# Kernel optimization log

Hardware: AMD Instinct MI355X
Metric: run time of the kernel (lower is better)

Reference implementation:

```python
import jax, jax.numpy as jnp
import numpy as np

B, L, D = 2, 256, 256


def setup_inputs() -> dict:
    key = jax.random.key(0)
    k1, k2, k3, k4 = jax.random.split(key, 4)
    x = jax.random.normal(k1, (B, L, D), dtype=jnp.float32)
    # nn.Linear(dim, 2*dim, bias=False): weight (2*dim, dim), out = x @ W.T
    W_a = jax.random.normal(k2, (2 * D, D), dtype=jnp.float32) / np.sqrt(D).astype(np.float32)
    # last_hidden_init: complex (dim,) parameter, split into real/imag floats
    h0_real = jax.random.normal(k3, (D,), dtype=jnp.float32)
    h0_imag = jax.random.normal(k4, (D,), dtype=jnp.float32)
    return {"x": x, "W_a": W_a, "h0_real": h0_real, "h0_imag": h0_imag}


def reference(x, W_a, h0_real, h0_imag):
    b, l, d = x.shape
    # a = view_as_complex(linear_a(x).float().view(b, l, d, 2))
    raw = (x.astype(jnp.float32) @ W_a.T).reshape(b, l, d, 2)
    re, im = raw[..., 0], raw[..., 1]
    mag2 = re * re + im * im                       # |a|^2
    a = jax.lax.complex(re, im) * (jax.lax.rsqrt(mag2) * jnp.exp(-mag2))
    a_ln = jnp.log(a)                              # (b, l, d) complex
    a_ln = jnp.transpose(a_ln, (0, 2, 1))          # (b, d, l)

    ii = jnp.arange(l)[:, None]
    kk = jnp.arange(l)[None, :]
    # a_ln_tri[b,d,i,k] = a_ln[b,d,k] if k >= i else 0 (== .triu())
    tri = jnp.where(kk >= ii, a_ln[:, :, None, :], 0.0)   # (b, d, l, l)
    # FFT causal conv with ones(len,len) row == cumulative sum along k
    cum = jnp.cumsum(tri, axis=-1)
    # c[b,d,i,k] = exp(sum_{j=i}^{k} a_ln_j) for k>=i, 1 at k=i-1, 0 below (.triu(-1))
    c = jnp.where(kk >= ii - 1, jnp.exp(cum), 0.0)         # (b, d, l, l)

    xT = jnp.transpose(x.astype(jnp.complex64), (0, 2, 1))  # (b, d, l)
    x_hat = jnp.roll(xT, 1, axis=2)                          # x_hat[k] = x[k-1]
    h0 = jax.lax.complex(h0_real, h0_imag)                   # (d,)
    x_hat = x_hat.at[:, :, 0].set(jnp.broadcast_to(h0, (b, d)))
    # x_mat does not depend on i, so (x_mat * c).sum(3) == einsum over k
    h = jnp.einsum('bdik,bdk->bdi', c, x_hat)
    h = h.at[:, :, -1].add(xT[:, :, -1])
    return jnp.transpose(h.real, (0, 2, 1)).astype(x.dtype)  # (b, l, d)
```

## Files before the change

kernel.cpp:

```cpp
#include <hip/hip_runtime.h>
#include <hip/hip_bf16.h>


constexpr int B = 2, L = 256, D = 256, K = 256;
constexpr int LT = 4;

__global__ __launch_bounds__(256) void gemm_a_kernel(
    const float* __restrict__ x,
    const float* __restrict__ W,
    float2* __restrict__ a)
{
    const int blk = blockIdx.x;
    const int b  = blk / (L / LT);
    const int l0 = (blk % (L / LT)) * LT;
    const int d  = threadIdx.x;

    __shared__ float xs[LT][K];

    const float4* src = (const float4*)(x + (size_t)(b * L + l0) * K);
    ((float4*)&xs[0][0])[d] = src[d];
    __syncthreads();

    const float4* w0 = (const float4*)(W + (size_t)(2 * d) * K);
    const float4* w1 = (const float4*)(W + (size_t)(2 * d + 1) * K);

    float accr[LT] = {0.f, 0.f, 0.f, 0.f};
    float acci[LT] = {0.f, 0.f, 0.f, 0.f};

#pragma unroll 4
    for (int k = 0; k < K / 4; ++k) {
        const float4 v0 = w0[k];
        const float4 v1 = w1[k];
#pragma unroll
        for (int r = 0; r < LT; ++r) {
            const float4 xv = ((const float4*)&xs[r][0])[k];
            accr[r] += v0.x * xv.x + v0.y * xv.y + v0.z * xv.z + v0.w * xv.w;
            acci[r] += v1.x * xv.x + v1.y * xv.y + v1.z * xv.z + v1.w * xv.w;
        }
    }

#pragma unroll
    for (int r = 0; r < LT; ++r) {
        const float re = accr[r], im = acci[r];
        const float m2 = re * re + im * im;
        const float s  = rsqrtf(m2) * expf(-m2);
        a[(size_t)(b * L + l0 + r) * D + d] = make_float2(re * s, im * s);
    }
}

__global__ __launch_bounds__(256) void scan_h_kernel(
    const float* __restrict__ x,
    const float2* __restrict__ a,
    const float* __restrict__ h0r,
    const float* __restrict__ h0i,
    float* __restrict__ out)
{
    const int b = blockIdx.x >> 8;
    const int d = blockIdx.x & 255;
    const int i = threadIdx.x;

    __shared__ float2 As[L];
    __shared__ float2 Bs[L];

    const size_t col = (size_t)b * L * D + d;

    const float2 ai = a[col + (size_t)i * D];
    float xr, xi;
    if (i == 0) { xr = h0r[d]; xi = h0i[d]; }
    else        { xr = x[col + (size_t)(i - 1) * D]; xi = 0.f; }

    float Ar = ai.x, Ai = ai.y;
    float Br = ai.x * xr - ai.y * xi;
    float Bi = ai.x * xi + ai.y * xr;

#pragma unroll
    for (int o = 1; o < L; o <<= 1) {
        As[i] = make_float2(Ar, Ai);
        Bs[i] = make_float2(Br, Bi);
        __syncthreads();
        if (i + o < L) {
            const float2 An = As[i + o];
            const float2 Bn = Bs[i + o];
            const float nAr = Ar * An.x - Ai * An.y;
            const float nAi = Ar * An.y + Ai * An.x;
            const float nBr = Ar * Bn.x - Ai * Bn.y + Br;
            const float nBi = Ar * Bn.y + Ai * Bn.x + Bi;
            Ar = nAr; Ai = nAi; Br = nBr; Bi = nBi;
        }
        __syncthreads();
    }

    float o_val = Br;
    if (i >= 2)      o_val += x[col + (size_t)(i - 2) * D];
    else if (i == 1) o_val += h0r[d];
    if (i == L - 1)  o_val += x[col + (size_t)(L - 1) * D];
    out[col + (size_t)i * D] = o_val;
}

extern "C" void kernel_launch(void* const* d_in, const int* in_sizes, int n_in,
                              void* d_out, int out_size, void* d_ws, size_t ws_size,
                              hipStream_t stream) {
    const float* x    = (const float*)d_in[0];
    const float* W_a  = (const float*)d_in[1];
    const float* h0r  = (const float*)d_in[2];
    const float* h0i  = (const float*)d_in[3];
    float* out = (float*)d_out;
    float2* a  = (float2*)d_ws;

    gemm_a_kernel<<<dim3(B * (L / LT)), dim3(256), 0, stream>>>(x, W_a, a);
    scan_h_kernel<<<dim3(B * D), dim3(256), 0, stream>>>(x, a, h0r, h0i, out);
}
```

Before: 82.52 us.

## Retile linear GEMM into 16x16 output tiles with shared-memory W and x

The projection GEMM moves from one thread per output column reading W rows straight from global memory to 2D tiles: each block stages 16 rows of x and 32 rows of W in padded shared memory, and each thread computes one complex output. The grid grows from 128 to 512 blocks, which improves occupancy and removes the uncoalesced per-thread W streaming. In exchange each thread does less register reuse, and shared memory per block rises to about 50KB.

```diff
diff --git a/kernel.cpp b/kernel.cpp
--- a/kernel.cpp
+++ b/kernel.cpp
@@ -3,49 +3,62 @@
 
 
 constexpr int B = 2, L = 256, D = 256, K = 256;
-constexpr int LT = 4;
+constexpr int TL = 16;
+constexpr int TD = 16;
+constexpr int PAD = 260;
 
 __global__ __launch_bounds__(256) void gemm_a_kernel(
     const float* __restrict__ x,
     const float* __restrict__ W,
     float2* __restrict__ a)
 {
-    const int blk = blockIdx.x;
-    const int b  = blk / (L / LT);
-    const int l0 = (blk % (L / LT)) * LT;
-    const int d  = threadIdx.x;
+    const int dt = blockIdx.x;
+    const int lt = blockIdx.y;
+    const int b  = blockIdx.z;
+    const int t  = threadIdx.x;
+    const int l0 = lt * TL;
+    const int d0 = dt * TD;
+    const int r0 = 2 * d0;
 
-    __shared__ float xs[LT][K];
+    __shared__ float xs[TL][PAD];
+    __shared__ float ws[2 * TD][PAD];
 
-    const float4* src = (const float4*)(x + (size_t)(b * L + l0) * K);
-    ((float4*)&xs[0][0])[d] = src[d];
+    {
+        const float4* src = (const float4*)(x + (size_t)(b * L + l0) * K);
+#pragma unroll
+        for (int j = 0; j < 4; ++j) {
+            const int g = j * 256 + t;
+            const int row = g >> 6, c4 = g & 63;
+            *(float4*)&xs[row][c4 * 4] = src[g];
+        }
+    }
+    {
+        const float4* src = (const float4*)(W + (size_t)r0 * K);
+#pragma unroll
+        for (int j = 0; j < 8; ++j) {
+            const int g = j * 256 + t;
+            const int row = g >> 6, c4 = g & 63;
+            *(float4*)&ws[row][c4 * 4] = src[g];
+        }
+    }
     __syncthreads();
 
-    const float4* w0 = (const float4*)(W + (size_t)(2 * d) * K);
-    const float4* w1 = (const float4*)(W + (size_t)(2 * d + 1) * K);
+    const int l  = t >> 4;
+    const int dd = t & 15;
 
-    float accr[LT] = {0.f, 0.f, 0.f, 0.f};
-    float acci[LT] = {0.f, 0.f, 0.f, 0.f};
-
-#pragma unroll 4
-    for (int k = 0; k < K / 4; ++k) {
-        const float4 v0 = w0[k];
-        const float4 v1 = w1[k];
-#pragma unroll
-        for (int r = 0; r < LT; ++r) {
-            const float4 xv = ((const float4*)&xs[r][0])[k];
-            accr[r] += v0.x * xv.x + v0.y * xv.y + v0.z * xv.z + v0.w * xv.w;
-            acci[r] += v1.x * xv.x + v1.y * xv.y + v1.z * xv.z + v1.w * xv.w;
-        }
+    float re = 0.f, im = 0.f;
+#pragma unroll 8
+    for (int k4 = 0; k4 < K / 4; ++k4) {
+        const float4 xv = *(const float4*)&xs[l][k4 * 4];
+        const float4 w0 = *(const float4*)&ws[2 * dd][k4 * 4];
+        const float4 w1 = *(const float4*)&ws[2 * dd + 1][k4 * 4];
+        re += xv.x * w0.x + xv.y * w0.y + xv.z * w0.z + xv.w * w0.w;
+        im += xv.x * w1.x + xv.y * w1.y + xv.z * w1.z + xv.w * w1.w;
     }
 
-#pragma unroll
-    for (int r = 0; r < LT; ++r) {
-        const float re = accr[r], im = acci[r];
-        const float m2 = re * re + im * im;
-        const float s  = rsqrtf(m2) * expf(-m2);
-        a[(size_t)(b * L + l0 + r) * D + d] = make_float2(re * s, im * s);
-    }
+    const float m2 = re * re + im * im;
+    const float s  = rsqrtf(m2) * expf(-m2);
+    a[(size_t)(b * L + l0 + l) * D + d0 + dd] = make_float2(re * s, im * s);
 }
 
 __global__ __launch_bounds__(256) void scan_h_kernel(
@@ -107,6 +120,6 @@
     float* out = (float*)d_out;
     float2* a  = (float2*)d_ws;
 
-    gemm_a_kernel<<<dim3(B * (L / LT)), dim3(256), 0, stream>>>(x, W_a, a);
+    gemm_a_kernel<<<dim3(D / TD, L / TL, B), dim3(256), 0, stream>>>(x, W_a, a);
     scan_h_kernel<<<dim3(B * D), dim3(256), 0, stream>>>(x, a, h0r, h0i, out);
 }
```

Result: faster. 71.87 us (-12.9%).

## Fuse projection GEMM and complex scan into a single kernel

Applied to the files above, without the earlier changes.

Merges the linear projection and the associative complex scan into one kernel. Each 512-thread block computes the projection for two feature columns across all positions, then scans them in shared memory. This removes the workspace round-trip for the intermediate a and one kernel launch, and packs the scan state into one float4 array. In exchange, every thread reads a full row of x from global memory with a stride of K between threads, so x is re-read once per feature pair with no shared tiling. The grid also shrinks to 256 blocks.

```diff
diff --git a/kernel.cpp b/kernel.cpp
--- a/kernel.cpp
+++ b/kernel.cpp
@@ -3,98 +3,72 @@
 
 
 constexpr int B = 2, L = 256, D = 256, K = 256;
-constexpr int LT = 4;
 
-__global__ __launch_bounds__(256) void gemm_a_kernel(
+__global__ __launch_bounds__(512) void sioconv_fused_kernel(
     const float* __restrict__ x,
     const float* __restrict__ W,
-    float2* __restrict__ a)
-{
-    const int blk = blockIdx.x;
-    const int b  = blk / (L / LT);
-    const int l0 = (blk % (L / LT)) * LT;
-    const int d  = threadIdx.x;
-
-    __shared__ float xs[LT][K];
-
-    const float4* src = (const float4*)(x + (size_t)(b * L + l0) * K);
-    ((float4*)&xs[0][0])[d] = src[d];
-    __syncthreads();
-
-    const float4* w0 = (const float4*)(W + (size_t)(2 * d) * K);
-    const float4* w1 = (const float4*)(W + (size_t)(2 * d + 1) * K);
-
-    float accr[LT] = {0.f, 0.f, 0.f, 0.f};
-    float acci[LT] = {0.f, 0.f, 0.f, 0.f};
-
-#pragma unroll 4
-    for (int k = 0; k < K / 4; ++k) {
-        const float4 v0 = w0[k];
-        const float4 v1 = w1[k];
-#pragma unroll
-        for (int r = 0; r < LT; ++r) {
-            const float4 xv = ((const float4*)&xs[r][0])[k];
-            accr[r] += v0.x * xv.x + v0.y * xv.y + v0.z * xv.z + v0.w * xv.w;
-            acci[r] += v1.x * xv.x + v1.y * xv.y + v1.z * xv.z + v1.w * xv.w;
-        }
-    }
-
-#pragma unroll
-    for (int r = 0; r < LT; ++r) {
-        const float re = accr[r], im = acci[r];
-        const float m2 = re * re + im * im;
-        const float s  = rsqrtf(m2) * expf(-m2);
-        a[(size_t)(b * L + l0 + r) * D + d] = make_float2(re * s, im * s);
-    }
-}
-
-__global__ __launch_bounds__(256) void scan_h_kernel(
-    const float* __restrict__ x,
-    const float2* __restrict__ a,
     const float* __restrict__ h0r,
     const float* __restrict__ h0i,
     float* __restrict__ out)
 {
-    const int b = blockIdx.x >> 8;
-    const int d = blockIdx.x & 255;
-    const int i = threadIdx.x;
+    const int b  = blockIdx.x >> 7;
+    const int dp = blockIdx.x & 127;
+    const int t  = threadIdx.x;
+    const int c  = t >> 8;
+    const int l  = t & 255;
+    const int d  = 2 * dp + c;
 
-    __shared__ float2 As[L];
-    __shared__ float2 Bs[L];
+    const float4* x4 = (const float4*)(x + (size_t)(b * L + l) * K);
+    const float4* w4 = (const float4*)(W + (size_t)(2 * d) * K);
 
-    const size_t col = (size_t)b * L * D + d;
+    float re = 0.f, im = 0.f;
+#pragma unroll 8
+    for (int k4 = 0; k4 < K / 4; ++k4) {
+        const float4 xv = x4[k4];
+        const float4 w0 = w4[k4];
+        const float4 w1 = w4[k4 + 64];
+        re += xv.x * w0.x + xv.y * w0.y + xv.z * w0.z + xv.w * w0.w;
+        im += xv.x * w1.x + xv.y * w1.y + xv.z * w1.z + xv.w * w1.w;
+    }
 
-    const float2 ai = a[col + (size_t)i * D];
+    const float m2 = re * re + im * im;
+    const float s  = rsqrtf(m2) * expf(-m2);
+    const float ar = re * s, ai = im * s;
+
+    __shared__ float4 Ms[2][L];
+    __shared__ float  xcol[2][L];
+
+    const size_t colbase = (size_t)b * L * D + d;
+
     float xr, xi;
-    if (i == 0) { xr = h0r[d]; xi = h0i[d]; }
-    else        { xr = x[col + (size_t)(i - 1) * D]; xi = 0.f; }
+    if (l == 0) { xr = h0r[d]; xi = h0i[d]; }
+    else        { xr = x[colbase + (size_t)(l - 1) * D]; xi = 0.f; }
+    xcol[c][l] = xr;
 
-    float Ar = ai.x, Ai = ai.y;
-    float Br = ai.x * xr - ai.y * xi;
-    float Bi = ai.x * xi + ai.y * xr;
+    float Ar = ar, Ai = ai;
+    float Br = ar * xr - ai * xi;
+    float Bi = ar * xi + ai * xr;
 
 #pragma unroll
     for (int o = 1; o < L; o <<= 1) {
-        As[i] = make_float2(Ar, Ai);
-        Bs[i] = make_float2(Br, Bi);
+        Ms[c][l] = make_float4(Ar, Ai, Br, Bi);
         __syncthreads();
-        if (i + o < L) {
-            const float2 An = As[i + o];
-            const float2 Bn = Bs[i + o];
-            const float nAr = Ar * An.x - Ai * An.y;
-            const float nAi = Ar * An.y + Ai * An.x;
-            const float nBr = Ar * Bn.x - Ai * Bn.y + Br;
-            const float nBi = Ar * Bn.y + Ai * Bn.x + Bi;
+        if (l + o < L) {
+            const float4 n = Ms[c][l + o];
+            const float nAr = Ar * n.x - Ai * n.y;
+            const float nAi = Ar * n.y + Ai * n.x;
+            const float nBr = Ar * n.z - Ai * n.w + Br;
+            const float nBi = Ar * n.w + Ai * n.z + Bi;
             Ar = nAr; Ai = nAi; Br = nBr; Bi = nBi;
         }
         __syncthreads();
     }
 
     float o_val = Br;
-    if (i >= 2)      o_val += x[col + (size_t)(i - 2) * D];
-    else if (i == 1) o_val += h0r[d];
-    if (i == L - 1)  o_val += x[col + (size_t)(L - 1) * D];
-    out[col + (size_t)i * D] = o_val;
+    if (l >= 2)      o_val += xcol[c][l - 1];
+    else if (l == 1) o_val += h0r[d];
+    if (l == L - 1)  o_val += x[colbase + (size_t)(L - 1) * D];
+    out[colbase + (size_t)l * D] = o_val;
 }
 
 extern "C" void kernel_launch(void* const* d_in, const int* in_sizes, int n_in,
@@ -105,8 +79,8 @@
     const float* h0r  = (const float*)d_in[2];
     const float* h0i  = (const float*)d_in[3];
     float* out = (float*)d_out;
-    float2* a  = (float2*)d_ws;
+    (void)d_ws; (void)ws_size;
 
-    gemm_a_kernel<<<dim3(B * (L / LT)), dim3(256), 0, stream>>>(x, W_a, a);
-    scan_h_kernel<<<dim3(B * D), dim3(256), 0, stream>>>(x, a, h0r, h0i, out);
+    sioconv_fused_kernel<<<dim3(B * (D / 2)), dim3(512), 0, stream>>>(
+        x, W_a, h0r, h0i, out);
 }
```

After: 84.60 us. +2.5%, slower.
